# Kernel tuning notes

Measured on AMD Instinct MI355X. Metric: run time of the kernel, lower is better.

Reference implementation:

```python
import math
import jax, jax.numpy as jnp
import numpy as np

B, C_IN, H, W = 16, 384, 64, 64
CDIM, K, NSCALES, ITERS = 128, 64, 2, 3

def conv1x1(x, w, b):
    # x: [B,C,H,W], w: [O,C], b: [O]
    return jnp.einsum('bchw,oc->bohw', x, w) + b[None, :, None, None]

def mlp2(x, w1, b1, w2, b2):
    return conv1x1(jax.nn.relu(conv1x1(x, w1, b1)), w2, b2)

def log_optimal_transport(scores, dustbin, iters):
    B_, K_, N_ = scores.shape
    Z = jnp.concatenate([scores, dustbin], axis=1)  # [B,K+1,N]
    log_mu = jnp.full((B_, K_ + 1), -math.log(K_ + 1), dtype=scores.dtype)
    log_nu = jnp.full((B_, N_), -math.log(N_), dtype=scores.dtype)
    u = jnp.zeros_like(log_mu)
    v = jnp.zeros_like(log_nu)
    for _ in range(iters):
        u = log_mu - jax.nn.logsumexp(Z + v[:, None, :], axis=2)
        v = log_nu - jax.nn.logsumexp(Z + u[:, :, None], axis=1)
    return Z + u[:, :, None] + v[:, None, :]

def avg_pool2(x):
    b, c, h, w = x.shape
    return x.reshape(b, c, h // 2, 2, w // 2, 2).mean(axis=(3, 5))

def scale_branch(xs, fw1, fb1, fw2, fb2, sw1, sb1, sw2, sb2, dw1, db1, dw2, db2):
    b = xs.shape[0]
    local_feat = mlp2(xs, fw1, fb1, fw2, fb2).reshape(b, CDIM, -1)   # [B,C,N]
    score = mlp2(xs, sw1, sb1, sw2, sb2).reshape(b, K, -1)           # [B,K,N]
    dustbin = mlp2(xs, dw1, db1, dw2, db2).reshape(b, 1, -1)         # [B,1,N]
    log_p = log_optimal_transport(score, dustbin, ITERS)
    p = jnp.exp(log_p)[:, :-1, :]                                    # drop dustbin row
    p = p / (p.sum(axis=-1, keepdims=True) + 1e-8)
    out = jnp.einsum('bcn,bkn->bck', local_feat, p)                  # [B,C,K]
    out = out / jnp.clip(jnp.linalg.norm(out, axis=1, keepdims=True), 1e-12)
    return out.reshape(b, -1), local_feat

def setup_inputs():
    key = jax.random.key(0)
    ks = jax.random.split(key, 13)
    inp = {'x': jax.random.normal(ks[0], (B, C_IN, H, W), jnp.float32)}
    kidx = 1
    for s in range(NSCALES):
        for name, (o, i) in [('fw1', (512, C_IN)), ('fw2', (CDIM, 512)),
                              ('sw1', (512, C_IN)), ('sw2', (K, 512)),
                              ('dw1', (128, C_IN)), ('dw2', (1, 128))]:
            inp[f'{name}_{s}'] = 0.02 * jax.random.normal(ks[kidx % 13], (o, i), jnp.float32)
            inp[f'{name[0]}b{name[2]}_{s}'] = jnp.zeros((o,), jnp.float32)
            kidx += 1
    return inp

def reference(x,
              fw1_0, fb1_0, fw2_0, fb2_0, sw1_0, sb1_0, sw2_0, sb2_0, dw1_0, db1_0, dw2_0, db2_0,
              fw1_1, fb1_1, fw2_1, fb2_1, sw1_1, sb1_1, sw2_1, sb2_1, dw1_1, db1_1, dw2_1, db2_1):
    params = [
        (fw1_0, fb1_0, fw2_0, fb2_0, sw1_0, sb1_0, sw2_0, sb2_0, dw1_0, db1_0, dw2_0, db2_0),
        (fw1_1, fb1_1, fw2_1, fb2_1, sw1_1, sb1_1, sw2_1, sb2_1, dw1_1, db1_1, dw2_1, db2_1),
    ]
    descs = []
    xs = x
    for s in range(NSCALES):
        if s > 0:
            xs = avg_pool2(xs)
        d, _ = scale_branch(xs, *params[s])
        descs.append(d)
    g = jnp.stack(descs, axis=1).mean(axis=1)
    g = g / jnp.clip(jnp.linalg.norm(g, axis=1, keepdims=True), 1e-12)
    return g
```

## Files before the change

### kernel.cpp

```cpp
#include <hip/hip_runtime.h>
#include <math.h>

typedef __attribute__((ext_vector_type(8))) short short8;
typedef __attribute__((ext_vector_type(4))) float floatx4;

__device__ inline float bf2f(short s) {
    union { unsigned u; float f; } x; x.u = ((unsigned)(unsigned short)s) << 16; return x.f;
}
__device__ inline short f2bf(float f) {
    union { float f; unsigned u; } x; x.f = f;
    unsigned r = x.u + 0x7fff + ((x.u >> 16) & 1);
    return (short)(r >> 16);
}

struct WSet {
    const float *fw1, *fb1, *fw2, *sw1, *sb1, *sw2, *sb2, *dw1, *db1, *dw2, *db2;
};

__device__ inline void wprep_core(const WSet A,
    short* __restrict__ W1f, short* __restrict__ W2af, short* __restrict__ W2bf,
    float* __restrict__ B1p, float* __restrict__ B2bp, int id)
{
    if (id < 491520) {
        int e = id & 7, l = (id >> 3) & 63, g = (id >> 9) & 15, rest = id >> 13;
        int kc = rest % 12, c = rest / 12;
        int m = c * 256 + g * 16 + (l & 15);
        int k = kc * 32 + (l >> 4) * 8 + e;
        float v = 0.f;
        if (m < 512) v = A.fw1[m * 384 + k];
        else if (m < 1024) v = A.sw1[(m - 512) * 384 + k];
        else if (m < 1152) v = A.dw1[(m - 1024) * 384 + k];
        W1f[id] = f2bf(v);
        return;
    }
    id -= 491520;
    if (id < 65536) {
        int e = id & 7, l = (id >> 3) & 63, g = (id >> 9) & 7, ka = id >> 12;
        int r = g * 16 + (l & 15), k = ka * 32 + (l >> 4) * 8 + e;
        W2af[id] = f2bf(A.fw2[r * 512 + k]);
        return;
    }
    id -= 65536;
    if (id < 98304) {
        int e = id & 7, l = (id >> 3) & 63, g = (id >> 9) & 7, kb = id >> 12;
        int r = g * 16 + (l & 15), krel = kb * 32 + (l >> 4) * 8 + e;
        float v = 0.f;
        if (r < 64 && krel < 512) v = A.sw2[r * 512 + krel];
        else if (r == 64 && krel >= 512 && krel < 640) v = A.dw2[krel - 512];
        W2bf[id] = f2bf(v);
        return;
    }
    id -= 98304;
    if (id < 1280) {
        float v = 0.f;
        if (id < 512) v = A.fb1[id];
        else if (id < 1024) v = A.sb1[id - 512];
        else if (id < 1152) v = A.db1[id - 1024];
        B1p[id] = v;
        return;
    }
    id -= 1280;
    if (id < 128) B2bp[id] = id < 64 ? A.sb2[id] : id == 64 ? A.db2[0] : 0.f;
}

__device__ inline void xprep_core(const float* __restrict__ x,
                                  short* __restrict__ xT, short* __restrict__ x1T,
                                  float* xt, int ip, int cg, int b, int t)
{
    #pragma unroll
    for (int u = 0; u < 8; u++) {
        int idx = t + 256 * u;
        int c = idx >> 5, spq = idx & 31;
        float4 v = *(const float4*)&x[(((long)b * 384 + cg * 64 + c) * 64 + ip * 2 + (spq >> 4)) * 64 + (spq & 15) * 4];
        float* d = &xt[c * 129 + spq * 4];
        d[0] = v.x; d[1] = v.y; d[2] = v.z; d[3] = v.w;
    }
    __syncthreads();
    {
        int sp = t >> 1, ch = t & 1;
        short tmp[32];
        #pragma unroll
        for (int cc = 0; cc < 32; cc++) tmp[cc] = f2bf(xt[(ch * 32 + cc) * 129 + sp]);
        short* dst = xT + ((long)b * 4096 + ip * 128 + sp) * 384 + cg * 64 + ch * 32;
        #pragma unroll
        for (int v = 0; v < 4; v++) *(short8*)(dst + v * 8) = *(short8*)(tmp + v * 8);
    }
    {
        int j1 = t >> 3, c8 = t & 7;
        short tmp[8];
        #pragma unroll
        for (int e = 0; e < 8; e++) {
            int c = c8 * 8 + e;
            float v = 0.25f * (xt[c * 129 + j1 * 2]      + xt[c * 129 + j1 * 2 + 1] +
                               xt[c * 129 + 64 + j1 * 2] + xt[c * 129 + 64 + j1 * 2 + 1]);
            tmp[e] = f2bf(v);
        }
        *(short8*)(x1T + ((long)b * 1024 + ip * 32 + j1) * 384 + cg * 64 + c8 * 8) = *(short8*)tmp;
    }
}

__global__ __launch_bounds__(256) void wprep(WSet a0, WSet a1,
    short* __restrict__ W1f, short* __restrict__ W2af, short* __restrict__ W2bf,
    float* __restrict__ B1p, float* __restrict__ B2bp)
{
    const int s = blockIdx.y;
    const WSet A = s ? a1 : a0;
    wprep_core(A, W1f + (size_t)s * 491520, W2af + (size_t)s * 65536,
               W2bf + (size_t)s * 98304, B1p + s * 1280, B2bp + s * 128,
               blockIdx.x * 256 + threadIdx.x);
}

__global__ __launch_bounds__(256) void xprep(const float* __restrict__ x,
                                             short* __restrict__ xT, short* __restrict__ x1T)
{
    __shared__ float xt[64 * 129];
    xprep_core(x, xT, x1T, xt, blockIdx.x, blockIdx.y, blockIdx.z, threadIdx.x);
}

__global__ __launch_bounds__(256) void prep(WSet a0, WSet a1,
    short* __restrict__ W1f, short* __restrict__ W2af, short* __restrict__ W2bf,
    float* __restrict__ B1p, float* __restrict__ B2bp,
    const float* __restrict__ x, short* __restrict__ xT, short* __restrict__ x1T)
{
    __shared__ float xt[64 * 129];
    const int bid = blockIdx.x, t = threadIdx.x;
    if (bid < 5132) {
        const int s = bid >= 2566;
        const WSet A = s ? a1 : a0;
        wprep_core(A, W1f + (size_t)s * 491520, W2af + (size_t)s * 65536,
                   W2bf + (size_t)s * 98304, B1p + s * 1280, B2bp + s * 128,
                   (bid - (s ? 2566 : 0)) * 256 + t);
    } else {
        const int xb = bid - 5132;
        xprep_core(x, xT, x1T, xt, xb & 31, (xb >> 5) % 6, (xb >> 5) / 6, t);
    }
}

__global__ __launch_bounds__(512, 4) void fused_mlp(
    const short* __restrict__ W1f_, const float* __restrict__ B1p_,
    const short* __restrict__ W2af_, const float* __restrict__ fb2_0, const float* __restrict__ fb2_1,
    const short* __restrict__ W2bf_, const float* __restrict__ B2bp_,
    const short* __restrict__ xT, const short* __restrict__ x1T,
    float* __restrict__ feat0, float* __restrict__ feat1,
    short* __restrict__ Eg0, short* __restrict__ Eg1,
    float* __restrict__ pu0, float* __restrict__ pu1)
{
    __shared__ short xs[12 * 2048];
    __shared__ short hs[8 * 2048];
    const int tid = threadIdx.x;
    const int wid = tid >> 6, lane = tid & 63;
    const int l15 = lane & 15, q = lane >> 4;
    const int mg = wid >> 1, ng = wid & 1;
    const int bx = blockIdx.x, b = blockIdx.y;
    const int sc = bx >= 64;
    const int tile = sc ? bx - 64 : bx;
    const int N = sc ? 1024 : 4096;
    const int n0 = tile * 64;
    const short* XT = sc ? x1T : xT;
    const short* W1f = W1f_ + (size_t)sc * 491520;
    const float* B1p = B1p_ + sc * 1280;
    const short* W2af = W2af_ + (size_t)sc * 65536;
    const short* W2bf = W2bf_ + (size_t)sc * 98304;
    const float* fb2 = sc ? fb2_1 : fb2_0;
    const float* B2bp = B2bp_ + sc * 128;
    float* feat = (sc ? feat1 : feat0) + (long)b * 128 * N;
    short* Eg = (sc ? Eg1 : Eg0) + (long)b * 65 * N;
    float* pu = sc ? pu1 : pu0;
    const int npart = sc ? 16 : 64;

    {
        const int n = tid >> 3;
        const int c0 = (tid & 7) * 6;
        const short* src = XT + ((long)b * N + n0 + n) * 384 + c0 * 8;
        const int jj = n >> 4, nl = n & 15;
        #pragma unroll
        for (int i = 0; i < 6; i++) {
            int c = c0 + i;
            int kc = c >> 2, qq = c & 3;
            *(short8*)(xs + kc * 2048 + jj * 512 + ((qq << 4) | nl) * 8) =
                *(const short8*)(src + i * 8);
        }
    }
    __syncthreads();

    floatx4 acc2[2][4];
    #pragma unroll
    for (int i = 0; i < 2; i++)
        #pragma unroll
        for (int j = 0; j < 4; j++) acc2[i][j] = floatx4{0.f, 0.f, 0.f, 0.f};

    auto phase2 = [&](int pc) {
        if (pc < 2) {
            const short* WA = W2af + (size_t)pc * 32768;
            short8 hb[2][4], wa[2];
            #pragma unroll
            for (int j = 0; j < 4; j++) hb[0][j] = *(short8*)(hs + j * 512 + lane * 8);
            wa[0] = *(const short8*)(WA + wid * 512 + lane * 8);
            #pragma unroll
            for (int kc2 = 0; kc2 < 8; kc2++) {
                short8 bfr[4];
                #pragma unroll
                for (int j = 0; j < 4; j++) bfr[j] = hb[kc2 & 1][j];
                short8 aF = wa[kc2 & 1];
                if (kc2 + 1 < 8) {
                    #pragma unroll
                    for (int j = 0; j < 4; j++)
                        hb[(kc2 + 1) & 1][j] = *(short8*)(hs + (kc2 + 1) * 2048 + j * 512 + lane * 8);
                    wa[(kc2 + 1) & 1] = *(const short8*)(WA + ((kc2 + 1) * 8 + wid) * 512 + lane * 8);
                }
                #pragma unroll
                for (int j = 0; j < 4; j++)
                    acc2[0][j] = __builtin_amdgcn_mfma_f32_16x16x32_bf16(aF, bfr[j], acc2[0][j], 0, 0, 0);
            }
        } else {
            if (wid >= 5) return;
            const short* WB = W2bf + (size_t)(pc - 2) * 32768;
            short8 hb[2][4], we[2];
            #pragma unroll
            for (int j = 0; j < 4; j++) hb[0][j] = *(short8*)(hs + j * 512 + lane * 8);
            we[0] = *(const short8*)(WB + wid * 512 + lane * 8);
            #pragma unroll
            for (int kc2 = 0; kc2 < 8; kc2++) {
                short8 bfr[4];
                #pragma unroll
                for (int j = 0; j < 4; j++) bfr[j] = hb[kc2 & 1][j];
                short8 aE = we[kc2 & 1];
                if (kc2 + 1 < 8) {
                    #pragma unroll
                    for (int j = 0; j < 4; j++)
                        hb[(kc2 + 1) & 1][j] = *(short8*)(hs + (kc2 + 1) * 2048 + j * 512 + lane * 8);
                    we[(kc2 + 1) & 1] = *(const short8*)(WB + ((kc2 + 1) * 8 + wid) * 512 + lane * 8);
                }
                #pragma unroll
                for (int j = 0; j < 4; j++)
                    acc2[1][j] = __builtin_amdgcn_mfma_f32_16x16x32_bf16(aE, bfr[j], acc2[1][j], 0, 0, 0);
            }
        }
    };

    for (int c = 0; c < 5; c++) {
        if (c > 0) phase2(c - 1);
        floatx4 acc1[4][2];
        #pragma unroll
        for (int i = 0; i < 4; i++)
            #pragma unroll
            for (int j = 0; j < 2; j++) acc1[i][j] = floatx4{0.f, 0.f, 0.f, 0.f};
        const short* Wb = W1f + (long)c * 98304;
        short8 abuf[2][4];
        #pragma unroll
        for (int i = 0; i < 4; i++) {
            abuf[0][i] = *(const short8*)(Wb + (mg * 4 + i) * 512 + lane * 8);
            abuf[1][i] = *(const short8*)(Wb + (16 + mg * 4 + i) * 512 + lane * 8);
        }
        #pragma unroll
        for (int kc = 0; kc < 12; kc++) {
            short8 ac[4], bc[2];
            #pragma unroll
            for (int i = 0; i < 4; i++) ac[i] = abuf[kc & 1][i];
            #pragma unroll
            for (int j = 0; j < 2; j++)
                bc[j] = *(short8*)(xs + kc * 2048 + (ng * 2 + j) * 512 + lane * 8);
            if (kc + 2 < 12) {
                #pragma unroll
                for (int i = 0; i < 4; i++)
                    abuf[kc & 1][i] = *(const short8*)(Wb + ((kc + 2) * 16 + mg * 4 + i) * 512 + lane * 8);
            }
            #pragma unroll
            for (int i = 0; i < 4; i++)
                #pragma unroll
                for (int j = 0; j < 2; j++)
                    acc1[i][j] = __builtin_amdgcn_mfma_f32_16x16x32_bf16(ac[i], bc[j], acc1[i][j], 0, 0, 0);
        }
        __syncthreads();
        #pragma unroll
        for (int i = 0; i < 4; i++) {
            const int kc2 = mg * 2 + (i >> 1);
            const int qf = (i & 1) * 2 + (q >> 1);
            const int e0 = 4 * (q & 1);
            const int mrow = c * 256 + mg * 64 + i * 16 + q * 4;
            float bw[4];
            #pragma unroll
            for (int rr = 0; rr < 4; rr++) bw[rr] = B1p[mrow + rr];
            #pragma unroll
            for (int j = 0; j < 2; j++) {
                const int jj = ng * 2 + j;
                short pk[4];
                #pragma unroll
                for (int rr = 0; rr < 4; rr++)
                    pk[rr] = f2bf(fmaxf(acc1[i][j][rr] + bw[rr], 0.f));
                *(unsigned long long*)(hs + kc2 * 2048 + jj * 512 + ((qf << 4) | l15) * 8 + e0) =
                    *(unsigned long long*)pk;
            }
        }
        __syncthreads();
    }
    phase2(4);

    {
        const int row0 = wid * 16 + q * 4;
        #pragma unroll
        for (int rr = 0; rr < 4; rr++) {
            float bv = fb2[row0 + rr];
            #pragma unroll
            for (int j = 0; j < 4; j++)
                feat[(long)(row0 + rr) * N + n0 + 16 * j + l15] = acc2[0][j][rr] + bv;
        }
    }
    __syncthreads();
    float* puld = (float*)hs;
    if (wid < 4) {
        #pragma unroll
        for (int rr = 0; rr < 4; rr++) {
            int row = wid * 16 + q * 4 + rr;
            float bv = B2bp[row];
            float s = 0.f;
            #pragma unroll
            for (int j = 0; j < 4; j++) {
                float e = expf(acc2[1][j][rr] + bv);
                Eg[(long)row * N + n0 + 16 * j + l15] = f2bf(e);
                s += e;
            }
            s += __shfl_xor(s, 1); s += __shfl_xor(s, 2);
            s += __shfl_xor(s, 4); s += __shfl_xor(s, 8);
            if (l15 == 0) puld[row] = s;
        }
    } else if (wid == 4) {
        #pragma unroll
        for (int rr = 0; rr < 4; rr++) {
            int row = 64 + q * 4 + rr;
            bool valid = (row == 64);
            float bv = B2bp[64];
            float s = 0.f;
            #pragma unroll
            for (int j = 0; j < 4; j++) {
                float e = expf(acc2[1][j][rr] + bv);
                if (valid) {
                    Eg[(long)64 * N + n0 + 16 * j + l15] = f2bf(e);
                    s += e;
                }
            }
            s += __shfl_xor(s, 1); s += __shfl_xor(s, 2);
            s += __shfl_xor(s, 4); s += __shfl_xor(s, 8);
            if (valid && l15 == 0) puld[64] = s;
        }
    }
    __syncthreads();
    if (tid < 65)
        pu[((long)b * npart + tile) * 65 + tid] = puld[tid];
}

__global__ __launch_bounds__(256) void sk_step(
    const short* __restrict__ Eg0, const short* __restrict__ Eg1,
    const float* __restrict__ pin0, const float* __restrict__ pin1,
    float* __restrict__ pout0, float* __restrict__ pout1, int nin0, int nin1)
{
    __shared__ short Es[65 * 264];
    __shared__ float evs[256];
    __shared__ float eus[65];
    const int t = threadIdx.x;
    const int bx = blockIdx.x, b = blockIdx.y;
    const int sc = bx >= 16;
    const int chunk = sc ? bx - 16 : bx;
    const int N = sc ? 1024 : 4096;
    const float invN = sc ? (1.0f / 1024.0f) : (1.0f / 4096.0f);
    const int n0 = chunk * 256;
    const short* Eb = (sc ? Eg1 : Eg0) + (long)b * 65 * N;
    const float* pin = sc ? pin1 : pin0;
    const int nin = sc ? nin1 : nin0;
    float* pout = sc ? pout1 : pout0;
    const int nout = sc ? 4 : 16;
    if (t < 65) {
        float s = 0.f;
        for (int ch = 0; ch < nin; ch++) s += pin[((long)b * nin + ch) * 65 + t];
        eus[t] = (1.0f / 65.0f) / s;
    }
    for (int it = t; it < 2080; it += 256) {
        int k = it >> 5, n8 = it & 31;
        *(short8*)(Es + k * 264 + n8 * 8) = *(const short8*)(Eb + (long)k * N + n0 + n8 * 8);
    }
    __syncthreads();
    float sv = 0.f;
    #pragma unroll 4
    for (int k = 0; k < 65; k++) sv += bf2f(Es[k * 264 + t]) * eus[k];
    evs[t] = invN / sv;
    __syncthreads();
    const int wid = t >> 6, lane = t & 63;
    for (int k = wid; k < 65; k += 4) {
        const short* er = Es + k * 264 + lane * 4;
        float4 v4 = *(const float4*)&evs[lane * 4];
        float s = bf2f(er[0]) * v4.x + bf2f(er[1]) * v4.y + bf2f(er[2]) * v4.z + bf2f(er[3]) * v4.w;
        #pragma unroll
        for (int off = 32; off >= 1; off >>= 1) s += __shfl_xor(s, off);
        if (lane == 0) pout[((long)b * nout + chunk) * 65 + k] = s;
    }
}

__global__ __launch_bounds__(256) void sk_desc(
    const short* __restrict__ Eg0, const short* __restrict__ Eg1,
    const float* __restrict__ pin0, const float* __restrict__ pin1,
    const float* __restrict__ feat0, const float* __restrict__ feat1,
    float* __restrict__ part0, float* __restrict__ part1, int nin0, int nin1)
{
    __shared__ short Es[65 * 264];
    __shared__ float eus[65];
    __shared__ float evs[256];
    const int t = threadIdx.x;
    const int bx = blockIdx.x, b = blockIdx.y;
    const int sc = bx >= 16;
    const int chunk = sc ? bx - 16 : bx;
    const int N = sc ? 1024 : 4096;
    const float invN = sc ? (1.0f / 1024.0f) : (1.0f / 4096.0f);
    const int nch = sc ? 4 : 16;
    const int n0 = chunk * 256;
    const short* Eb = (sc ? Eg1 : Eg0) + (long)b * 65 * N;
    const float* pin = sc ? pin1 : pin0;
    const int nin = sc ? nin1 : nin0;
    const float* fb = (sc ? feat1 : feat0) + (long)b * 128 * N;
    float* part = sc ? part1 : part0;
    if (t < 65) {
        float s = 0.f;
        for (int ch = 0; ch < nin; ch++) s += pin[((long)b * nin + ch) * 65 + t];
        eus[t] = (1.0f / 65.0f) / s;
    }
    for (int it = t; it < 2080; it += 256) {
        int k = it >> 5, n8 = it & 31;
        *(short8*)(Es + k * 264 + n8 * 8) = *(const short8*)(Eb + (long)k * N + n0 + n8 * 8);
    }
    __syncthreads();
    float sv = 0.f;
    #pragma unroll 4
    for (int k = 0; k < 65; k++) sv += bf2f(Es[k * 264 + t]) * eus[k];
    evs[t] = invN / sv;
    __syncthreads();
    const int wid = t >> 6, lane = t & 63;
    const int l15 = lane & 15, q = lane >> 4;
    float* pb = part + ((long)b * nch + chunk) * 8256;
    for (int k = wid; k < 64; k += 4) {
        const short* er = Es + k * 264 + lane * 4;
        float4 v4 = *(const float4*)&evs[lane * 4];
        float s = bf2f(er[0]) * v4.x + bf2f(er[1]) * v4.y + bf2f(er[2]) * v4.z + bf2f(er[3]) * v4.w;
        #pragma unroll
        for (int off = 32; off >= 1; off >>= 1) s += __shfl_xor(s, off);
        if (lane == 0) pb[8192 + k] = s * eus[k];
    }
    floatx4 acc[2][4];
    #pragma unroll
    for (int mt = 0; mt < 2; mt++)
        #pragma unroll
        for (int nt = 0; nt < 4; nt++) acc[mt][nt] = floatx4{0.f, 0.f, 0.f, 0.f};
    #pragma unroll 2
    for (int ks = 0; ks < 8; ks++) {
        float4 ev0 = *(const float4*)&evs[ks * 32 + q * 8];
        float4 ev1 = *(const float4*)&evs[ks * 32 + q * 8 + 4];
        float evq[8] = {ev0.x, ev0.y, ev0.z, ev0.w, ev1.x, ev1.y, ev1.z, ev1.w};
        short8 ah[2], al[2];
        #pragma unroll
        for (int mt = 0; mt < 2; mt++) {
            const float* fp = fb + (long)(wid * 32 + mt * 16 + l15) * N + n0 + ks * 32 + q * 8;
            float4 v0 = *(const float4*)fp;
            float4 v1 = *(const float4*)(fp + 4);
            float va[8] = {v0.x, v0.y, v0.z, v0.w, v1.x, v1.y, v1.z, v1.w};
            short hh[8], ll[8];
            #pragma unroll
            for (int e = 0; e < 8; e++) {
                float sv2 = va[e] * evq[e];
                short h = f2bf(sv2);
                hh[e] = h;
                ll[e] = f2bf(sv2 - bf2f(h));
            }
            ah[mt] = *(short8*)hh;
            al[mt] = *(short8*)ll;
        }
        #pragma unroll
        for (int nt = 0; nt < 4; nt++) {
            short8 bfr = *(short8*)(Es + (nt * 16 + l15) * 264 + ks * 32 + q * 8);
            #pragma unroll
            for (int mt = 0; mt < 2; mt++) {
                acc[mt][nt] = __builtin_amdgcn_mfma_f32_16x16x32_bf16(al[mt], bfr, acc[mt][nt], 0, 0, 0);
                acc[mt][nt] = __builtin_amdgcn_mfma_f32_16x16x32_bf16(ah[mt], bfr, acc[mt][nt], 0, 0, 0);
            }
        }
    }
    #pragma unroll
    for (int nt = 0; nt < 4; nt++) {
        float euk = eus[nt * 16 + l15];
        #pragma unroll
        for (int mt = 0; mt < 2; mt++)
            #pragma unroll
            for (int rr = 0; rr < 4; rr++)
                pb[(wid * 32 + mt * 16 + q * 4 + rr) * 64 + nt * 16 + l15] = acc[mt][nt][rr] * euk;
    }
}

__global__ __launch_bounds__(256) void desc_reduce(
    const float* __restrict__ part0, const float* __restrict__ part1,
    float* __restrict__ desc0, float* __restrict__ desc1, int b0)
{
    __shared__ float cred[4][8];
    const int bx = blockIdx.x, b = blockIdx.y;
    const int sc = bx >= 4;
    const int kg = (bx & 3) * 16;
    const int nch = sc ? 4 : 16;
    const float* pb = (sc ? part1 : part0) + (long)b * nch * 8256;
    float* desc = sc ? desc1 : desc0;
    const int t = threadIdx.x;
    const int c = t & 127, kh = t >> 7;
    float a[8], rs[8];
    #pragma unroll
    for (int j = 0; j < 8; j++) { a[j] = 0.f; rs[j] = 0.f; }
    for (int ch = 0; ch < nch; ch++) {
        const float* p = pb + (long)ch * 8256;
        #pragma unroll
        for (int j = 0; j < 8; j++) a[j] += p[c * 64 + kg + kh * 8 + j];
        #pragma unroll
        for (int j = 0; j < 8; j++) rs[j] += p[8192 + kg + kh * 8 + j];
    }
    float sq[8];
    #pragma unroll
    for (int j = 0; j < 8; j++) {
        a[j] *= 1.0f / (rs[j] + 1e-8f);
        sq[j] = a[j] * a[j];
    }
    #pragma unroll
    for (int off = 32; off >= 1; off >>= 1)
        #pragma unroll
        for (int j = 0; j < 8; j++) sq[j] += __shfl_xor(sq[j], off);
    if ((t & 63) == 0) {
        #pragma unroll
        for (int j = 0; j < 8; j++) cred[t >> 6][j] = sq[j];
    }
    __syncthreads();
    float* d = desc + (long)(b0 + b) * 8192;
    #pragma unroll
    for (int j = 0; j < 8; j++) {
        float tot = cred[kh * 2][j] + cred[kh * 2 + 1][j];
        float inv = 1.0f / fmaxf(sqrtf(tot), 1e-12f);
        d[c * 64 + kg + kh * 8 + j] = a[j] * inv;
    }
}

__global__ __launch_bounds__(256) void final_kernel(const float* __restrict__ desc0,
                                                    const float* __restrict__ desc1,
                                                    float* __restrict__ out)
{
    __shared__ float red[4];
    const int b = blockIdx.x;
    const float* d0 = desc0 + (long)b * 8192;
    const float* d1 = desc1 + (long)b * 8192;
    float s = 0;
    for (int i = threadIdx.x; i < 8192; i += 256) {
        float t = (d0[i] + d1[i]) * 0.5f; s += t * t;
    }
    const int wave = threadIdx.x >> 6, lane = threadIdx.x & 63;
    #pragma unroll
    for (int off = 32; off >= 1; off >>= 1) s += __shfl_xor(s, off);
    if (lane == 0) red[wave] = s;
    __syncthreads();
    float tot = red[0] + red[1] + red[2] + red[3];
    float inv = 1.0f / fmaxf(sqrtf(tot), 1e-12f);
    for (int i = threadIdx.x; i < 8192; i += 256)
        out[(long)b * 8192 + i] = (d0[i] + d1[i]) * 0.5f * inv;
}

extern "C" void kernel_launch(void* const* d_in, const int* in_sizes, int n_in,
                              void* d_out, int out_size, void* d_ws, size_t ws_size,
                              hipStream_t stream)
{
    (void)in_sizes; (void)n_in; (void)out_size;
    const float* x = (const float*)d_in[0];
    WSet ws2[2];
    const float* fb2p[2];
    for (int s = 0; s < 2; s++) {
        int o = 1 + s * 12;
        ws2[s].fw1 = (const float*)d_in[o + 0];  ws2[s].fb1 = (const float*)d_in[o + 1];
        ws2[s].fw2 = (const float*)d_in[o + 2];  fb2p[s]    = (const float*)d_in[o + 3];
        ws2[s].sw1 = (const float*)d_in[o + 4];  ws2[s].sb1 = (const float*)d_in[o + 5];
        ws2[s].sw2 = (const float*)d_in[o + 6];  ws2[s].sb2 = (const float*)d_in[o + 7];
        ws2[s].dw1 = (const float*)d_in[o + 8];  ws2[s].db1 = (const float*)d_in[o + 9];
        ws2[s].dw2 = (const float*)d_in[o + 10]; ws2[s].db2 = (const float*)d_in[o + 11];
    }

    const size_t fixed = ((size_t)2*491520*2 + 2*65536*2 + 2*98304*2
                        + 2*1280*4 + 2*128*4 + (size_t)2*16*8192*4) + (1 << 16);
    const size_t perb = (size_t)4096*384*2 + (size_t)1024*384*2
                      + (size_t)128*4096*4 + (size_t)128*1024*4
                      + (size_t)65*4096*2 + (size_t)65*1024*2
                      + (size_t)(64+16)*65*4 + (size_t)(16+4)*65*4
                      + (size_t)16*8256*4 + (size_t)4*8256*4 + 8192;
    int CB = 4;
    const int cand[3] = {16, 8, 4};
    for (int ci = 0; ci < 3; ci++)
        if (fixed + (size_t)cand[ci] * perb <= ws_size) { CB = cand[ci]; break; }

    char* p = (char*)d_ws;
    auto alloc = [&](size_t bytes) -> char* {
        char* r = p; p += (bytes + 255) & ~(size_t)255; return r;
    };
    short* W1f   = (short*)alloc((size_t)2 * 491520 * 2);
    short* W2af  = (short*)alloc((size_t)2 * 65536 * 2);
    short* W2bf  = (short*)alloc((size_t)2 * 98304 * 2);
    float* B1p   = (float*)alloc((size_t)2 * 1280 * 4);
    float* B2bp  = (float*)alloc((size_t)2 * 128 * 4);
    float* desc0 = (float*)alloc((size_t)16 * 8192 * 4);
    float* desc1 = (float*)alloc((size_t)16 * 8192 * 4);
    short* xT    = (short*)alloc((size_t)CB * 4096 * 384 * 2);
    short* x1T   = (short*)alloc((size_t)CB * 1024 * 384 * 2);
    float* feat0 = (float*)alloc((size_t)CB * 128 * 4096 * 4);
    float* feat1 = (float*)alloc((size_t)CB * 128 * 1024 * 4);
    short* Eg0   = (short*)alloc((size_t)CB * 65 * 4096 * 2);
    short* Eg1   = (short*)alloc((size_t)CB * 65 * 1024 * 2);
    float* puA0  = (float*)alloc((size_t)CB * 64 * 65 * 4);
    float* puA1  = (float*)alloc((size_t)CB * 16 * 65 * 4);
    float* puB0  = (float*)alloc((size_t)CB * 16 * 65 * 4);
    float* puB1  = (float*)alloc((size_t)CB * 4 * 65 * 4);
    float* part0 = (float*)alloc((size_t)CB * 16 * 8256 * 4);
    float* part1 = (float*)alloc((size_t)CB * 4 * 8256 * 4);

    if (CB == 16) {
        prep<<<dim3(8204), 256, 0, stream>>>(ws2[0], ws2[1],
            W1f, W2af, W2bf, B1p, B2bp, x, xT, x1T);
        fused_mlp<<<dim3(80, 16), 512, 0, stream>>>(
            W1f, B1p, W2af, fb2p[0], fb2p[1], W2bf, B2bp,
            xT, x1T, feat0, feat1, Eg0, Eg1, puA0, puA1);
        sk_step<<<dim3(20, 16), 256, 0, stream>>>(Eg0, Eg1, puA0, puA1, puB0, puB1, 64, 16);
        sk_step<<<dim3(20, 16), 256, 0, stream>>>(Eg0, Eg1, puB0, puB1, puA0, puA1, 16, 4);
        sk_desc<<<dim3(20, 16), 256, 0, stream>>>(Eg0, Eg1, puA0, puA1,
                                                  feat0, feat1, part0, part1, 16, 4);
        desc_reduce<<<dim3(8, 16), 256, 0, stream>>>(part0, part1, desc0, desc1, 0);
        final_kernel<<<16, 256, 0, stream>>>(desc0, desc1, (float*)d_out);
    } else {
        wprep<<<dim3(2566, 2), 256, 0, stream>>>(ws2[0], ws2[1], W1f, W2af, W2bf, B1p, B2bp);
        for (int b0 = 0; b0 < 16; b0 += CB) {
            xprep<<<dim3(32, 6, CB), 256, 0, stream>>>(x + (size_t)b0 * 384 * 4096, xT, x1T);
            fused_mlp<<<dim3(80, CB), 512, 0, stream>>>(
                W1f, B1p, W2af, fb2p[0], fb2p[1], W2bf, B2bp,
                xT, x1T, feat0, feat1, Eg0, Eg1, puA0, puA1);
            sk_step<<<dim3(20, CB), 256, 0, stream>>>(Eg0, Eg1, puA0, puA1, puB0, puB1, 64, 16);
            sk_step<<<dim3(20, CB), 256, 0, stream>>>(Eg0, Eg1, puB0, puB1, puA0, puA1, 16, 4);
            sk_desc<<<dim3(20, CB), 256, 0, stream>>>(Eg0, Eg1, puA0, puA1,
                                                      feat0, feat1, part0, part1, 16, 4);
            desc_reduce<<<dim3(8, CB), 256, 0, stream>>>(part0, part1, desc0, desc1, b0);
        }
        final_kernel<<<16, 256, 0, stream>>>(desc0, desc1, (float*)d_out);
    }
}
```

Baseline: 455.0 us.

## Re-tile first MLP GEMM per wave and fuse descriptor reduce with final normalize

The first-layer GEMM in fused_mlp now gives each of the 8 waves 2 M-tiles by all 4 N-tiles instead of 4 by 2. Each wave therefore issues fewer global weight loads and more LDS activation reads, and writes its ReLU output into a single hs k-chunk. The desc_reduce and final_kernel launches are merged into one dred_final kernel per batch. It sums the partials, applies the row-sum and per-cluster L2 normalisation in LDS, averages the two scales and writes the output directly, which drops one launch and the desc buffers. The merged kernel runs only 16 blocks with about 66KB of LDS each, so the reduction step has less parallelism.

```diff
diff --git a/kernel.cpp b/kernel.cpp
--- a/kernel.cpp
+++ b/kernel.cpp
@@ -150,7 +150,6 @@
     const int tid = threadIdx.x;
     const int wid = tid >> 6, lane = tid & 63;
     const int l15 = lane & 15, q = lane >> 4;
-    const int mg = wid >> 1, ng = wid & 1;
     const int bx = blockIdx.x, b = blockIdx.y;
     const int sc = bx >= 64;
     const int tile = sc ? bx - 64 : bx;
@@ -240,55 +239,52 @@
 
     for (int c = 0; c < 5; c++) {
         if (c > 0) phase2(c - 1);
-        floatx4 acc1[4][2];
-        #pragma unroll
-        for (int i = 0; i < 4; i++)
-            #pragma unroll
-            for (int j = 0; j < 2; j++) acc1[i][j] = floatx4{0.f, 0.f, 0.f, 0.f};
+        floatx4 acc1[2][4];
+        #pragma unroll
+        for (int i = 0; i < 2; i++)
+            #pragma unroll
+            for (int j = 0; j < 4; j++) acc1[i][j] = floatx4{0.f, 0.f, 0.f, 0.f};
         const short* Wb = W1f + (long)c * 98304;
-        short8 abuf[2][4];
-        #pragma unroll
-        for (int i = 0; i < 4; i++) {
-            abuf[0][i] = *(const short8*)(Wb + (mg * 4 + i) * 512 + lane * 8);
-            abuf[1][i] = *(const short8*)(Wb + (16 + mg * 4 + i) * 512 + lane * 8);
+        short8 abuf[2][2];
+        #pragma unroll
+        for (int i = 0; i < 2; i++) {
+            abuf[0][i] = *(const short8*)(Wb + (wid * 2 + i) * 512 + lane * 8);
+            abuf[1][i] = *(const short8*)(Wb + (16 + wid * 2 + i) * 512 + lane * 8);
         }
         #pragma unroll
         for (int kc = 0; kc < 12; kc++) {
-            short8 ac[4], bc[2];
-            #pragma unroll
-            for (int i = 0; i < 4; i++) ac[i] = abuf[kc & 1][i];
-            #pragma unroll
-            for (int j = 0; j < 2; j++)
-                bc[j] = *(short8*)(xs + kc * 2048 + (ng * 2 + j) * 512 + lane * 8);
+            short8 ac[2], bc[4];
+            #pragma unroll
+            for (int i = 0; i < 2; i++) ac[i] = abuf[kc & 1][i];
+            #pragma unroll
+            for (int j = 0; j < 4; j++) bc[j] = *(short8*)(xs + kc * 2048 + j * 512 + lane * 8);
             if (kc + 2 < 12) {
                 #pragma unroll
-                for (int i = 0; i < 4; i++)
-                    abuf[kc & 1][i] = *(const short8*)(Wb + ((kc + 2) * 16 + mg * 4 + i) * 512 + lane * 8);
-            }
-            #pragma unroll
-            for (int i = 0; i < 4; i++)
+                for (int i = 0; i < 2; i++)
+                    abuf[kc & 1][i] = *(const short8*)(Wb + ((kc + 2) * 16 + wid * 2 + i) * 512 + lane * 8);
+            }
+            #pragma unroll
+            for (int i = 0; i < 2; i++)
                 #pragma unroll
-                for (int j = 0; j < 2; j++)
+                for (int j = 0; j < 4; j++)
                     acc1[i][j] = __builtin_amdgcn_mfma_f32_16x16x32_bf16(ac[i], bc[j], acc1[i][j], 0, 0, 0);
         }
         __syncthreads();
         #pragma unroll
-        for (int i = 0; i < 4; i++) {
-            const int kc2 = mg * 2 + (i >> 1);
-            const int qf = (i & 1) * 2 + (q >> 1);
+        for (int i = 0; i < 2; i++) {
+            const int qf = i * 2 + (q >> 1);
             const int e0 = 4 * (q & 1);
-            const int mrow = c * 256 + mg * 64 + i * 16 + q * 4;
+            const int mrow = c * 256 + wid * 32 + i * 16 + q * 4;
             float bw[4];
             #pragma unroll
             for (int rr = 0; rr < 4; rr++) bw[rr] = B1p[mrow + rr];
             #pragma unroll
-            for (int j = 0; j < 2; j++) {
-                const int jj = ng * 2 + j;
+            for (int j = 0; j < 4; j++) {
                 short pk[4];
                 #pragma unroll
                 for (int rr = 0; rr < 4; rr++)
                     pk[rr] = f2bf(fmaxf(acc1[i][j][rr] + bw[rr], 0.f));
-                *(unsigned long long*)(hs + kc2 * 2048 + jj * 512 + ((qf << 4) | l15) * 8 + e0) =
+                *(unsigned long long*)(hs + wid * 2048 + j * 512 + ((qf << 4) | l15) * 8 + e0) =
                     *(unsigned long long*)pk;
             }
         }
@@ -492,74 +488,68 @@
     }
 }
 
-__global__ __launch_bounds__(256) void desc_reduce(
+__global__ __launch_bounds__(256) void dred_final(
     const float* __restrict__ part0, const float* __restrict__ part1,
-    float* __restrict__ desc0, float* __restrict__ desc1, int b0)
-{
-    __shared__ float cred[4][8];
-    const int bx = blockIdx.x, b = blockIdx.y;
-    const int sc = bx >= 4;
-    const int kg = (bx & 3) * 16;
-    const int nch = sc ? 4 : 16;
-    const float* pb = (sc ? part1 : part0) + (long)b * nch * 8256;
-    float* desc = sc ? desc1 : desc0;
-    const int t = threadIdx.x;
-    const int c = t & 127, kh = t >> 7;
-    float a[8], rs[8];
-    #pragma unroll
-    for (int j = 0; j < 8; j++) { a[j] = 0.f; rs[j] = 0.f; }
-    for (int ch = 0; ch < nch; ch++) {
-        const float* p = pb + (long)ch * 8256;
-        #pragma unroll
-        for (int j = 0; j < 8; j++) a[j] += p[c * 64 + kg + kh * 8 + j];
-        #pragma unroll
-        for (int j = 0; j < 8; j++) rs[j] += p[8192 + kg + kh * 8 + j];
-    }
-    float sq[8];
-    #pragma unroll
-    for (int j = 0; j < 8; j++) {
-        a[j] *= 1.0f / (rs[j] + 1e-8f);
-        sq[j] = a[j] * a[j];
-    }
-    #pragma unroll
-    for (int off = 32; off >= 1; off >>= 1)
-        #pragma unroll
-        for (int j = 0; j < 8; j++) sq[j] += __shfl_xor(sq[j], off);
-    if ((t & 63) == 0) {
-        #pragma unroll
-        for (int j = 0; j < 8; j++) cred[t >> 6][j] = sq[j];
-    }
-    __syncthreads();
-    float* d = desc + (long)(b0 + b) * 8192;
-    #pragma unroll
-    for (int j = 0; j < 8; j++) {
-        float tot = cred[kh * 2][j] + cred[kh * 2 + 1][j];
-        float inv = 1.0f / fmaxf(sqrtf(tot), 1e-12f);
-        d[c * 64 + kg + kh * 8 + j] = a[j] * inv;
-    }
-}
-
-__global__ __launch_bounds__(256) void final_kernel(const float* __restrict__ desc0,
-                                                    const float* __restrict__ desc1,
-                                                    float* __restrict__ out)
-{
+    float* __restrict__ out, int b0)
+{
+    __shared__ float d0s[128 * 65];
+    __shared__ float d1s[128 * 65];
+    __shared__ float rsv[64];
     __shared__ float red[4];
     const int b = blockIdx.x;
-    const float* d0 = desc0 + (long)b * 8192;
-    const float* d1 = desc1 + (long)b * 8192;
-    float s = 0;
-    for (int i = threadIdx.x; i < 8192; i += 256) {
-        float t = (d0[i] + d1[i]) * 0.5f; s += t * t;
-    }
-    const int wave = threadIdx.x >> 6, lane = threadIdx.x & 63;
+    const int t = threadIdx.x;
+    const int c = t >> 1, k0 = (t & 1) * 32;
+
+    #pragma unroll
+    for (int s = 0; s < 2; s++) {
+        const int nch = s ? 4 : 16;
+        const float* pb = (s ? part1 : part0) + (long)b * nch * 8256;
+        float* ds = s ? d1s : d0s;
+        if (t < 64) {
+            float rs = 0.f;
+            for (int ch = 0; ch < nch; ch++) rs += pb[ch * 8256 + 8192 + t];
+            rsv[t] = 1.0f / (rs + 1e-8f);
+        }
+        __syncthreads();
+        float a[32];
+        #pragma unroll 8
+        for (int j = 0; j < 32; j++) a[j] = 0.f;
+        for (int ch = 0; ch < nch; ch++) {
+            const float* p = pb + ch * 8256 + c * 64 + k0;
+            #pragma unroll 8
+            for (int j = 0; j < 32; j++) a[j] += p[j];
+        }
+        #pragma unroll 8
+        for (int j = 0; j < 32; j++) ds[c * 65 + k0 + j] = a[j] * rsv[k0 + j];
+        __syncthreads();
+        if (t < 64) {
+            float sq = 0.f;
+            for (int c2 = 0; c2 < 128; c2++) { float v = ds[c2 * 65 + t]; sq += v * v; }
+            rsv[t] = 1.0f / fmaxf(sqrtf(sq), 1e-12f);
+        }
+        __syncthreads();
+        #pragma unroll 8
+        for (int j = 0; j < 32; j++) ds[c * 65 + k0 + j] *= rsv[k0 + j];
+        __syncthreads();
+    }
+    float s = 0.f;
+    for (int i = t; i < 8192; i += 256) {
+        int cc = i >> 6, k = i & 63;
+        float v = (d0s[cc * 65 + k] + d1s[cc * 65 + k]) * 0.5f;
+        s += v * v;
+    }
+    const int wave = t >> 6, lane = t & 63;
     #pragma unroll
     for (int off = 32; off >= 1; off >>= 1) s += __shfl_xor(s, off);
     if (lane == 0) red[wave] = s;
     __syncthreads();
     float tot = red[0] + red[1] + red[2] + red[3];
     float inv = 1.0f / fmaxf(sqrtf(tot), 1e-12f);
-    for (int i = threadIdx.x; i < 8192; i += 256)
-        out[(long)b * 8192 + i] = (d0[i] + d1[i]) * 0.5f * inv;
+    float* o = out + (long)(b0 + b) * 8192;
+    for (int i = t; i < 8192; i += 256) {
+        int cc = i >> 6, k = i & 63;
+        o[i] = (d0s[cc * 65 + k] + d1s[cc * 65 + k]) * 0.5f * inv;
+    }
 }
 
 extern "C" void kernel_launch(void* const* d_in, const int* in_sizes, int n_in,
@@ -581,7 +571,7 @@
     }
 
     const size_t fixed = ((size_t)2*491520*2 + 2*65536*2 + 2*98304*2
-                        + 2*1280*4 + 2*128*4 + (size_t)2*16*8192*4) + (1 << 16);
+                        + 2*1280*4 + 2*128*4) + (1 << 16);
     const size_t perb = (size_t)4096*384*2 + (size_t)1024*384*2
                       + (size_t)128*4096*4 + (size_t)128*1024*4
                       + (size_t)65*4096*2 + (size_t)65*1024*2
@@ -601,8 +591,6 @@
     short* W2bf  = (short*)alloc((size_t)2 * 98304 * 2);
     float* B1p   = (float*)alloc((size_t)2 * 1280 * 4);
     float* B2bp  = (float*)alloc((size_t)2 * 128 * 4);
-    float* desc0 = (float*)alloc((size_t)16 * 8192 * 4);
-    float* desc1 = (float*)alloc((size_t)16 * 8192 * 4);
     short* xT    = (short*)alloc((size_t)CB * 4096 * 384 * 2);
     short* x1T   = (short*)alloc((size_t)CB * 1024 * 384 * 2);
     float* feat0 = (float*)alloc((size_t)CB * 128 * 4096 * 4);
@@ -626,8 +614,7 @@
         sk_step<<<dim3(20, 16), 256, 0, stream>>>(Eg0, Eg1, puB0, puB1, puA0, puA1, 16, 4);
         sk_desc<<<dim3(20, 16), 256, 0, stream>>>(Eg0, Eg1, puA0, puA1,
                                                   feat0, feat1, part0, part1, 16, 4);
-        desc_reduce<<<dim3(8, 16), 256, 0, stream>>>(part0, part1, desc0, desc1, 0);
-        final_kernel<<<16, 256, 0, stream>>>(desc0, desc1, (float*)d_out);
+        dred_final<<<dim3(16), 256, 0, stream>>>(part0, part1, (float*)d_out, 0);
     } else {
         wprep<<<dim3(2566, 2), 256, 0, stream>>>(ws2[0], ws2[1], W1f, W2af, W2bf, B1p, B2bp);
         for (int b0 = 0; b0 < 16; b0 += CB) {
@@ -639,8 +626,7 @@
             sk_step<<<dim3(20, CB), 256, 0, stream>>>(Eg0, Eg1, puB0, puB1, puA0, puA1, 16, 4);
             sk_desc<<<dim3(20, CB), 256, 0, stream>>>(Eg0, Eg1, puA0, puA1,
                                                       feat0, feat1, part0, part1, 16, 4);
-            desc_reduce<<<dim3(8, CB), 256, 0, stream>>>(part0, part1, desc0, desc1, b0);
-        }
-        final_kernel<<<16, 256, 0, stream>>>(desc0, desc1, (float*)d_out);
-    }
-}
+            dred_final<<<dim3(CB), 256, 0, stream>>>(part0, part1, (float*)d_out, b0);
+        }
+    }
+}
```

Result: faster. 410.3 us (-9.8%).
